# Kernel optimization log

Hardware: AMD Instinct MI355X
Metric: run time of the kernel (lower is better)

Reference implementation:

```python
import jax, jax.numpy as jnp
import numpy as np

N, E, G = 50000, 400000, 2048
H, C = 4, 64            # heads, hidden per head
IN, ED, TASKS = 29, 6, 12
HC = H * C


def setup_inputs() -> dict:
    key = jax.random.key(0)
    ks = jax.random.split(key, 20)
    s = 0.1
    f32 = jnp.float32
    inp = {
        'x': jax.random.normal(ks[0], (N, IN), f32),
        'edge_index': jax.random.randint(ks[1], (2, E), 0, N),
        'edge_attr': jax.random.normal(ks[2], (E, ED), f32),
        'batch': jnp.sort(jax.random.randint(ks[3], (N,), 0, G)),
        # layer 1 (in=29 -> H*C=256)
        'W1': jax.random.normal(ks[4], (IN, HC), f32) * s,
        'as1': jax.random.normal(ks[5], (1, H, C), f32) * s,
        'ad1': jax.random.normal(ks[6], (1, H, C), f32) * s,
        'We1': jax.random.normal(ks[7], (ED, HC), f32) * s,
        'ae1': jax.random.normal(ks[8], (1, H, C), f32) * s,
        'b1': jnp.zeros((HC,), f32),
        # layer 2 (in=256 -> 256)
        'W2': jax.random.normal(ks[9], (HC, HC), f32) * s,
        'as2': jax.random.normal(ks[10], (1, H, C), f32) * s,
        'ad2': jax.random.normal(ks[11], (1, H, C), f32) * s,
        'We2': jax.random.normal(ks[12], (ED, HC), f32) * s,
        'ae2': jax.random.normal(ks[13], (1, H, C), f32) * s,
        'b2': jnp.zeros((HC,), f32),
        # readout linear (256 -> 12)
        'Wl': jax.random.normal(ks[14], (HC, TASKS), f32) * s,
        'bl': jnp.zeros((TASKS,), f32),
    }
    return inp


def _gat_conv(x, src, dst, eattr, W, a_src, a_dst, We, a_e, b):
    """PyG GATConv, concat=True, leaky_relu slope 0.2, self-loops already appended."""
    h = (x @ W).reshape(N, H, C)                      # [N,H,C]
    al_s = jnp.sum(h * a_src, axis=-1)                # [N,H]
    al_d = jnp.sum(h * a_dst, axis=-1)                # [N,H]
    he = (eattr @ We).reshape(-1, H, C)               # [Etot,H,C]
    al_e = jnp.sum(he * a_e, axis=-1)                 # [Etot,H]
    alpha = al_s[src] + al_d[dst] + al_e              # [Etot,H]
    alpha = jax.nn.leaky_relu(alpha, negative_slope=0.2)
    # segment softmax over incoming edges of each dst node
    amax = jax.ops.segment_max(alpha, dst, num_segments=N)
    ex = jnp.exp(alpha - amax[dst])
    denom = jax.ops.segment_sum(ex, dst, num_segments=N)
    alpha = ex / (denom[dst] + 1e-16)
    msg = h[src] * alpha[:, :, None]                  # [Etot,H,C]
    out = jax.ops.segment_sum(msg, dst, num_segments=N)
    return out.reshape(N, HC) + b


def reference(x, edge_index, edge_attr, batch,
              W1, as1, ad1, We1, ae1, b1,
              W2, as2, ad2, We2, ae2, b2, Wl, bl):
    # add self-loops with edge_attr fill = mean over existing edges (PyG default)
    loop = jnp.arange(N)
    src = jnp.concatenate([edge_index[0], loop])
    dst = jnp.concatenate([edge_index[1], loop])
    mean_e = jnp.mean(edge_attr, axis=0, keepdims=True)
    eattr = jnp.concatenate([edge_attr, jnp.broadcast_to(mean_e, (N, ED))], axis=0)

    h = _gat_conv(x, src, dst, eattr, W1, as1, ad1, We1, ae1, b1)
    h = jax.nn.relu(h)
    h = _gat_conv(h, src, dst, eattr, W2, as2, ad2, We2, ae2, b2)
    h = jax.nn.relu(h)

    # global mean pool over graphs
    sums = jax.ops.segment_sum(h, batch, num_segments=G)      # [G,HC]
    cnt = jax.ops.segment_sum(jnp.ones((N,), h.dtype), batch, num_segments=G)
    pooled = sums / jnp.maximum(cnt, 1.0)[:, None]
    return pooled @ Wl + bl
```

## Files before the change

kernel.cpp:

```cpp
#include <hip/hip_runtime.h>
#include <math.h>

static constexpr int NN = 50000;
static constexpr int EE = 400000;
static constexpr int GG = 2048;
static constexpr int TASKS = 12;

typedef __attribute__((ext_vector_type(8))) short short8;
typedef __attribute__((ext_vector_type(4))) float floatx4;

__device__ __forceinline__ unsigned short f2bf(float f) {
  unsigned u = __float_as_uint(f);
  u = u + 0x7fffu + ((u >> 16) & 1u);
  return (unsigned short)(u >> 16);
}
__device__ __forceinline__ float bflo(unsigned u) { return __uint_as_float(u << 16); }
__device__ __forceinline__ float bfhi(unsigned u) { return __uint_as_float(u & 0xffff0000u); }

static constexpr int NBDEG = (EE + 255) / 256;
static constexpr int NBMEAN = 256;
static constexpr int NBX = (NN * 4 + 255) / 256;
static constexpr int NW1 = 32;
static constexpr int NW2 = 256;
__global__ void k_pre(const int* __restrict__ dst, const float* __restrict__ ea,
                      const float* __restrict__ x, const float* __restrict__ W1,
                      const float* __restrict__ W2, int* __restrict__ deg,
                      float* __restrict__ msum, unsigned short* __restrict__ xb,
                      unsigned short* __restrict__ w1t, unsigned short* __restrict__ w2t) {
  const int b = blockIdx.x;
  const int t = threadIdx.x;
  if (b < NBDEG) {
    int e = b * 256 + t;
    if (e < EE) atomicAdd(&deg[dst[e]], 1);
  } else if (b < NBDEG + NBMEAN) {
    float s[6] = {0, 0, 0, 0, 0, 0};
    for (int e = (b - NBDEG) * 256 + t; e < EE; e += NBMEAN * 256) {
#pragma unroll
      for (int d = 0; d < 6; d++) s[d] += ea[(size_t)e * 6 + d];
    }
    __shared__ float ls[6];
    if (t < 6) ls[t] = 0.f;
    __syncthreads();
#pragma unroll
    for (int d = 0; d < 6; d++) atomicAdd(&ls[d], s[d]);
    __syncthreads();
    if (t < 6) atomicAdd(&msum[t], ls[t]);
  } else if (b < NBDEG + NBMEAN + NBX) {
    int i = (b - NBDEG - NBMEAN) * 256 + t;
    if (i < NN * 4) {
      int n = i >> 2, seg = i & 3;
      unsigned short v[8];
#pragma unroll
      for (int j = 0; j < 8; j++) {
        int k = seg * 8 + j;
        v[j] = (k < 29) ? f2bf(x[(size_t)n * 29 + k]) : (unsigned short)0;
      }
      *(short8*)(xb + (size_t)n * 32 + seg * 8) = *(short8*)v;
    }
  } else if (b < NBDEG + NBMEAN + NBX + NW1) {
    int i = (b - NBDEG - NBMEAN - NBX) * 256 + t;
    int row = i >> 5, k = i & 31;
    unsigned short v = (k < 29) ? f2bf(W1[(size_t)k * 256 + row]) : (unsigned short)0;
    w1t[((row >> 4) * 4 + (k >> 3)) * 128 + (row & 15) * 8 + (k & 7)] = v;
  } else {
    int i = (b - NBDEG - NBMEAN - NBX - NW1) * 256 + t;
    int row = i >> 8, k = i & 255;
    w2t[((row >> 4) * 32 + (k >> 3)) * 128 + (row & 15) * 8 + (k & 7)] = f2bf(W2[(size_t)k * 256 + row]);
  }
}

static constexpr int NBS = (NN + 255) / 256;

__global__ void k_scan1(const int* __restrict__ deg, int* __restrict__ rowptr,
                        int* __restrict__ bsums, const float* __restrict__ We1,
                        const float* __restrict__ ae1, const float* __restrict__ We2,
                        const float* __restrict__ ae2, const float* __restrict__ msum,
                        float* __restrict__ p1, float* __restrict__ p2) {
  const int t = threadIdx.x;
  if (blockIdx.x >= NBS) {
    const int layer = blockIdx.x - NBS;
    const float* We = layer ? We2 : We1;
    const float* ae = layer ? ae2 : ae1;
    float* params = layer ? p2 : p1;
    __shared__ float vsh[24];
    if (t < 24) {
      int d = t >> 2, h = t & 3;
      float s = 0.f;
      for (int c = 0; c < 64; c++) s += We[d * 256 + h * 64 + c] * ae[h * 64 + c];
      vsh[t] = s;
      params[t] = s;
    }
    __syncthreads();
    if (t < 4) {
      float s = 0.f;
      const float invE = 1.0f / (float)EE;
#pragma unroll
      for (int d = 0; d < 6; d++) s += (msum[d] * invE) * vsh[d * 4 + t];
      params[24 + t] = s;
    }
    return;
  }
  __shared__ int sh[256];
  int i = blockIdx.x * 256 + t;
  int v = (i < NN) ? deg[i] : 0;
  sh[t] = v;
  __syncthreads();
  for (int off = 1; off < 256; off <<= 1) {
    int tv = (t >= off) ? sh[t - off] : 0;
    __syncthreads();
    sh[t] += tv;
    __syncthreads();
  }
  if (i < NN) rowptr[i] = sh[t] - v;
  if (t == 255) bsums[blockIdx.x] = sh[255];
}

__global__ void k_scan23(int* __restrict__ rowptr, const int* __restrict__ bsums, int nb) {
  __shared__ int sh[256];
  const int t = threadIdx.x;
  sh[t] = (t < nb) ? bsums[t] : 0;
  __syncthreads();
  for (int off = 1; off < 256; off <<= 1) {
    int tv = (t >= off) ? sh[t - off] : 0;
    __syncthreads();
    sh[t] += tv;
    __syncthreads();
  }
  const int add = (blockIdx.x == 0) ? 0 : sh[blockIdx.x - 1];
  int i = blockIdx.x * 256 + t;
  if (i < NN) rowptr[i] += add;
  if (i == 0) rowptr[NN] = EE;
}

template <int KP>
__device__ __forceinline__ void gemm_body(
    int bx, const unsigned short* __restrict__ A, const unsigned short* __restrict__ Bt,
    const float* __restrict__ a_s, const float* __restrict__ a_d,
    unsigned short* __restrict__ Y, float* __restrict__ als, float* __restrict__ ald, int M) {
  __shared__ __align__(16) unsigned short Ash[64 * KP];
  const int tid = threadIdx.x;
  const int lane = tid & 63;
  const int w = tid >> 6;
  const int l15 = lane & 15;
  const int quad = lane >> 4;
  const int row0 = bx * 64;

  constexpr int STEPS = (64 * KP * 2) / (256 * 16);
  {
    const char* Ab = (const char*)(A + (size_t)row0 * KP);
    uint4 stg[STEPS];
#pragma unroll
    for (int s = 0; s < STEPS; s++) stg[s] = *(const uint4*)(Ab + s * 4096 + tid * 16);
#pragma unroll
    for (int s = 0; s < STEPS; s++) {
      int o = s * 4096 + tid * 16;
      int row = o / (KP * 2);
      *(uint4*)((char*)Ash + (o ^ ((row & 7) << 4))) = stg[s];
    }
  }

  floatx4 acc[4][4];
#pragma unroll
  for (int i = 0; i < 4; i++)
#pragma unroll
    for (int j = 0; j < 4; j++) acc[i][j] = {0.f, 0.f, 0.f, 0.f};

  const unsigned short* pb[4];
#pragma unroll
  for (int j = 0; j < 4; j++)
    pb[j] = Bt + (size_t)((w * 4 + j) * (KP / 8) + quad) * 128 + l15 * 8;

  constexpr int NPH = KP / 32;
  short8 bfr[3][4];
#pragma unroll
  for (int j = 0; j < 4; j++) bfr[0][j] = *(const short8*)pb[j];
  if (NPH > 1) {
#pragma unroll
    for (int j = 0; j < 4; j++) {
      pb[j] += 512;
      bfr[1][j] = *(const short8*)pb[j];
    }
  }

  __syncthreads();

  auto ldA = [&](int ph, short8 (&dst)[4]) {
#pragma unroll
    for (int i = 0; i < 4; i++) {
      int lin = (i * 16 + l15) * (KP * 2) + ph * 64 + quad * 16;
      dst[i] = *(const short8*)((const char*)Ash + (lin ^ ((l15 & 7) << 4)));
    }
  };
  short8 af[2][4];
  ldA(0, af[0]);

#pragma unroll
  for (int ph = 0; ph < NPH; ph++) {
    if (ph + 2 < NPH) {
#pragma unroll
      for (int j = 0; j < 4; j++) {
        pb[j] += 512;
        bfr[(ph + 2) % 3][j] = *(const short8*)pb[j];
      }
    }
    if (ph + 1 < NPH) ldA(ph + 1, af[(ph + 1) & 1]);
#pragma unroll
    for (int i = 0; i < 4; i++)
#pragma unroll
      for (int j = 0; j < 4; j++)
        acc[i][j] = __builtin_amdgcn_mfma_f32_16x16x32_bf16(af[ph & 1][i], bfr[ph % 3][j], acc[i][j], 0, 0, 0);
  }
  float asc[4], adc[4];
#pragma unroll
  for (int j = 0; j < 4; j++) {
    asc[j] = a_s[w * 64 + j * 16 + l15];
    adc[j] = a_d[w * 64 + j * 16 + l15];
  }
#pragma unroll
  for (int i = 0; i < 4; i++) {
#pragma unroll
    for (int r = 0; r < 4; r++) {
      const int row = row0 + i * 16 + quad * 4 + r;
      unsigned ub[4];
      float hv[4];
#pragma unroll
      for (int j = 0; j < 4; j++) {
        ub[j] = f2bf(acc[i][j][r]);
        hv[j] = __uint_as_float(ub[j] << 16);
      }
      if (row < M) {
#pragma unroll
        for (int j = 0; j < 4; j++) Y[(size_t)row * 256 + w * 64 + j * 16 + l15] = (unsigned short)ub[j];
      }
      float ps = hv[0] * asc[0] + hv[1] * asc[1] + hv[2] * asc[2] + hv[3] * asc[3];
      float pd = hv[0] * adc[0] + hv[1] * adc[1] + hv[2] * adc[2] + hv[3] * adc[3];
#pragma unroll
      for (int off = 1; off < 16; off <<= 1) {
        ps += __shfl_xor(ps, off, 64);
        pd += __shfl_xor(pd, off, 64);
      }
      if (l15 == 0 && row < M) {
        als[row * 4 + w] = ps;
        ald[row * 4 + w] = pd;
      }
    }
  }
}

static constexpr int GB = (NN + 63) / 64;

__global__ __launch_bounds__(256, 2) void k_scatgemm1(
    const int* __restrict__ ei, const int* __restrict__ rowptr, int* __restrict__ cursor,
    int* __restrict__ csrc, const float* __restrict__ ea,
    const float* __restrict__ p1, const float* __restrict__ p2,
    float* __restrict__ ed1, float* __restrict__ ed2,
    const unsigned short* __restrict__ xb, const unsigned short* __restrict__ w1t,
    const float* __restrict__ as1, const float* __restrict__ ad1,
    unsigned short* __restrict__ hb, float* __restrict__ als, float* __restrict__ ald) {
  const int b = blockIdx.x;
  const int t = threadIdx.x;
  if (b < NBDEG) {
    int e = b * 256 + t;
    if (e >= EE) return;
    int s = ei[e];
    int d = ei[EE + e];
    int p = atomicAdd(&cursor[d], 1);
    int slot = rowptr[d] + p;
    csrc[slot] = s;
    float ed6[6];
#pragma unroll
    for (int d6 = 0; d6 < 6; d6++) ed6[d6] = ea[(size_t)e * 6 + d6];
    float c1[4] = {0.f, 0.f, 0.f, 0.f}, c2[4] = {0.f, 0.f, 0.f, 0.f};
#pragma unroll
    for (int h = 0; h < 4; h++) {
#pragma unroll
      for (int d6 = 0; d6 < 6; d6++) {
        c1[h] += ed6[d6] * p1[d6 * 4 + h];
        c2[h] += ed6[d6] * p2[d6 * 4 + h];
      }
    }
    *(float4*)(ed1 + (size_t)slot * 4) = make_float4(c1[0], c1[1], c1[2], c1[3]);
    *(float4*)(ed2 + (size_t)slot * 4) = make_float4(c2[0], c2[1], c2[2], c2[3]);
  } else {
    gemm_body<32>(b - NBDEG, xb, w1t, as1, ad1, hb, als, ald, NN);
  }
}

__global__ __launch_bounds__(256, 2) void k_gemm2(
    const unsigned short* __restrict__ A, const unsigned short* __restrict__ Bt,
    const float* __restrict__ a_s, const float* __restrict__ a_d,
    unsigned short* __restrict__ Y, float* __restrict__ als, float* __restrict__ ald) {
  gemm_body<256>(blockIdx.x, A, Bt, a_s, a_d, Y, als, ald, NN);
}

__device__ __forceinline__ float leaky02(float x) { return x > 0.f ? x : 0.2f * x; }

__global__ __launch_bounds__(256) void k_agg(
    const unsigned short* __restrict__ hinb, const float* __restrict__ als,
    const float* __restrict__ ald, const int* __restrict__ rowptr, const int* __restrict__ csrc,
    const float* __restrict__ edc, const float* __restrict__ params, const float* __restrict__ bias,
    unsigned short* __restrict__ houtb) {
  const int lane = threadIdx.x & 63;
  const int n = blockIdx.x * 4 + (threadIdx.x >> 6);
  if (n >= NN) return;
  const int half = lane >> 5;
  const int sl = lane & 31;
  const int head = sl >> 3;

  const float aldn = ald[n * 4 + head];
  float acc[8];
  float ssum;
  {
    float slg = leaky02(als[n * 4 + head] + aldn + params[24 + head]);
    float exs = __expf(slg);
    float wgt = (half == 0) ? exs : 0.f;
    ssum = wgt;
    uint4 uv = *(const uint4*)(hinb + (size_t)n * 256 + sl * 8);
    acc[0] = bflo(uv.x) * wgt;
    acc[1] = bfhi(uv.x) * wgt;
    acc[2] = bflo(uv.y) * wgt;
    acc[3] = bfhi(uv.y) * wgt;
    acc[4] = bflo(uv.z) * wgt;
    acc[5] = bfhi(uv.z) * wgt;
    acc[6] = bflo(uv.w) * wgt;
    acc[7] = bfhi(uv.w) * wgt;
  }
  const int end = rowptr[n + 1];
  int s = rowptr[n] + half;
  while (s < end) {
    int sid[4];
    float edv[4];
#pragma unroll
    for (int k = 0; k < 4; k++) {
      const int q = s + 2 * k;
      const bool v = q < end;
      const int idx = v ? q : end - 1;
      sid[k] = csrc[idx];
      edv[k] = v ? edc[(size_t)idx * 4 + head] : 0.f;
    }
    float alv[4];
#pragma unroll
    for (int k = 0; k < 4; k++) alv[k] = als[(size_t)sid[k] * 4 + head];
    uint4 r[4];
#pragma unroll
    for (int k = 0; k < 4; k++) {
      r[k] = make_uint4(0u, 0u, 0u, 0u);
      if (s + 2 * k < end) r[k] = *(const uint4*)(hinb + (size_t)sid[k] * 256 + sl * 8);
    }
#pragma unroll
    for (int k = 0; k < 4; k++) {
      const float ex = (s + 2 * k < end) ? __expf(leaky02(alv[k] + aldn + edv[k])) : 0.f;
      acc[0] += bflo(r[k].x) * ex;
      acc[1] += bfhi(r[k].x) * ex;
      acc[2] += bflo(r[k].y) * ex;
      acc[3] += bfhi(r[k].y) * ex;
      acc[4] += bflo(r[k].z) * ex;
      acc[5] += bfhi(r[k].z) * ex;
      acc[6] += bflo(r[k].w) * ex;
      acc[7] += bfhi(r[k].w) * ex;
      ssum += ex;
    }
    s += 8;
  }
#pragma unroll
  for (int j = 0; j < 8; j++) acc[j] += __shfl_xor(acc[j], 32, 64);
  ssum += __shfl_xor(ssum, 32, 64);
  if (half == 0) {
    const float inv = 1.f / (ssum + 1e-16f);
    float4 b0 = *(const float4*)(bias + sl * 8);
    float4 b1 = *(const float4*)(bias + sl * 8 + 4);
    const float bb[8] = {b0.x, b0.y, b0.z, b0.w, b1.x, b1.y, b1.z, b1.w};
    uint p[4];
#pragma unroll
    for (int j = 0; j < 4; j++) {
      float e0 = fmaxf(acc[2 * j] * inv + bb[2 * j], 0.f);
      float e1 = fmaxf(acc[2 * j + 1] * inv + bb[2 * j + 1], 0.f);
      p[j] = (uint)f2bf(e0) | ((uint)f2bf(e1) << 16);
    }
    *(uint4*)(houtb + (size_t)n * 256 + sl * 8) = make_uint4(p[0], p[1], p[2], p[3]);
  }
}

__global__ __launch_bounds__(256) void k_pool(const unsigned short* __restrict__ hb,
                                              const int* __restrict__ batch,
                                              const float* __restrict__ Wl,
                                              const float* __restrict__ bl,
                                              float* __restrict__ out) {
  int g = blockIdx.x;
  int t = threadIdx.x;
  int lo = 0, hi = NN;
  while (lo < hi) {
    int mid = (lo + hi) >> 1;
    if (batch[mid] < g) lo = mid + 1; else hi = mid;
  }
  int start = lo;
  hi = NN;
  while (lo < hi) {
    int mid = (lo + hi) >> 1;
    if (batch[mid] < g + 1) lo = mid + 1; else hi = mid;
  }
  int end = lo;
  const int mid2 = start + ((end - start) >> 1);
  __shared__ float sp[256], sq[256];
  {
    const int c = t & 127;
    const int hseg = t >> 7;
    const int a = hseg ? mid2 : start;
    const int b = hseg ? end : mid2;
    float s0 = 0.f, s1 = 0.f;
    for (int n2 = a; n2 < b; n2++) {
      uint u = ((const uint*)(hb + (size_t)n2 * 256))[c];
      s0 += bflo(u);
      s1 += bfhi(u);
    }
    float* dst = hseg ? sq : sp;
    dst[2 * c] = s0;
    dst[2 * c + 1] = s1;
  }
  __syncthreads();
  if (t < TASKS) {
    float invc = 1.f / fmaxf((float)(end - start), 1.f);
    float o = bl[t];
    for (int c = 0; c < 256; c++) o += (sp[c] + sq[c]) * invc * Wl[c * 12 + t];
    out[(size_t)g * 12 + t] = o;
  }
}

extern "C" void kernel_launch(void* const* d_in, const int* in_sizes, int n_in,
                              void* d_out, int out_size, void* d_ws, size_t ws_size,
                              hipStream_t stream) {
  const float* x = (const float*)d_in[0];
  const int* ei = (const int*)d_in[1];
  const float* ea = (const float*)d_in[2];
  const int* batch = (const int*)d_in[3];
  const float* W1 = (const float*)d_in[4];
  const float* as1 = (const float*)d_in[5];
  const float* ad1 = (const float*)d_in[6];
  const float* We1 = (const float*)d_in[7];
  const float* ae1 = (const float*)d_in[8];
  const float* b1 = (const float*)d_in[9];
  const float* W2 = (const float*)d_in[10];
  const float* as2 = (const float*)d_in[11];
  const float* ad2 = (const float*)d_in[12];
  const float* We2 = (const float*)d_in[13];
  const float* ae2 = (const float*)d_in[14];
  const float* b2 = (const float*)d_in[15];
  const float* Wl = (const float*)d_in[16];
  const float* bl = (const float*)d_in[17];
  float* out = (float*)d_out;

  char* ws = (char*)d_ws;
  size_t off = 0;
  auto take = [&](size_t bytes) -> char* {
    char* p = ws + off;
    off = (off + bytes + 255) & ~(size_t)255;
    return p;
  };
  float* msum = (float*)take(8 * 4);
  int* deg = (int*)take((size_t)NN * 4);
  int* cursor = (int*)take((size_t)NN * 4);
  size_t zero_end = off;
  int* rowptr = (int*)take((size_t)(NN + 1) * 4);
  int* bsums = (int*)take(256 * 4);
  int* csrc = (int*)take((size_t)EE * 4);
  float* ed1 = (float*)take((size_t)EE * 4 * 4);
  float* ed2 = (float*)take((size_t)EE * 4 * 4);
  float* p1 = (float*)take(32 * 4);
  float* p2 = (float*)take(32 * 4);
  float* als = (float*)take((size_t)NN * 4 * 4);
  float* ald = (float*)take((size_t)NN * 4 * 4);
  unsigned short* hb = (unsigned short*)take((size_t)NN * 256 * 2);
  unsigned short* ab = (unsigned short*)take((size_t)NN * 256 * 2);
  unsigned short* xb = (unsigned short*)take((size_t)NN * 32 * 2);
  unsigned short* w1t = (unsigned short*)take((size_t)256 * 32 * 2);
  unsigned short* w2t = (unsigned short*)take((size_t)256 * 256 * 2);
  (void)ws_size;

  hipMemsetAsync(ws, 0, zero_end, stream);

  k_pre<<<NBDEG + NBMEAN + NBX + NW1 + NW2, 256, 0, stream>>>(ei + EE, ea, x, W1, W2,
                                                              deg, msum, xb, w1t, w2t);
  k_scan1<<<NBS + 2, 256, 0, stream>>>(deg, rowptr, bsums, We1, ae1, We2, ae2, msum, p1, p2);
  k_scan23<<<NBS, 256, 0, stream>>>(rowptr, bsums, NBS);

  k_scatgemm1<<<NBDEG + GB, 256, 0, stream>>>(ei, rowptr, cursor, csrc, ea, p1, p2,
                                              ed1, ed2, xb, w1t, as1, ad1, hb, als, ald);

  k_agg<<<NN / 4, 256, 0, stream>>>(hb, als, ald, rowptr, csrc, ed1, p1, b1, ab);

  k_gemm2<<<GB, 256, 0, stream>>>(ab, w2t, as2, ad2, hb, als, ald);
  k_agg<<<NN / 4, 256, 0, stream>>>(hb, als, ald, rowptr, csrc, ed2, p2, b2, ab);

  k_pool<<<GG, 256, 0, stream>>>(ab, batch, Wl, bl, out);
}
```

Before: 286.8 us.

## Compute edge attention terms on the fly in aggregation instead of precomputing

The scatter kernel now stores a packed (source, original edge id) pair per CSR slot. It no longer projects edge attributes into per-slot per-head attention terms for both layers. The aggregation kernel loads the six raw edge-attribute floats by edge id and dots them with per-head projection parameters held in registers. This removes writing and re-reading two per-edge term arrays, but adds random-order gathers of the edge-attribute array in each aggregation pass and a little extra arithmetic per edge.

```diff
diff --git a/kernel.cpp b/kernel.cpp
--- a/kernel.cpp
+++ b/kernel.cpp
@@ -251,9 +251,7 @@
 
 __global__ __launch_bounds__(256, 2) void k_scatgemm1(
     const int* __restrict__ ei, const int* __restrict__ rowptr, int* __restrict__ cursor,
-    int* __restrict__ csrc, const float* __restrict__ ea,
-    const float* __restrict__ p1, const float* __restrict__ p2,
-    float* __restrict__ ed1, float* __restrict__ ed2,
+    int2* __restrict__ cse,
     const unsigned short* __restrict__ xb, const unsigned short* __restrict__ w1t,
     const float* __restrict__ as1, const float* __restrict__ ad1,
     unsigned short* __restrict__ hb, float* __restrict__ als, float* __restrict__ ald) {
@@ -266,21 +264,7 @@
     int d = ei[EE + e];
     int p = atomicAdd(&cursor[d], 1);
     int slot = rowptr[d] + p;
-    csrc[slot] = s;
-    float ed6[6];
-#pragma unroll
-    for (int d6 = 0; d6 < 6; d6++) ed6[d6] = ea[(size_t)e * 6 + d6];
-    float c1[4] = {0.f, 0.f, 0.f, 0.f}, c2[4] = {0.f, 0.f, 0.f, 0.f};
-#pragma unroll
-    for (int h = 0; h < 4; h++) {
-#pragma unroll
-      for (int d6 = 0; d6 < 6; d6++) {
-        c1[h] += ed6[d6] * p1[d6 * 4 + h];
-        c2[h] += ed6[d6] * p2[d6 * 4 + h];
-      }
-    }
-    *(float4*)(ed1 + (size_t)slot * 4) = make_float4(c1[0], c1[1], c1[2], c1[3]);
-    *(float4*)(ed2 + (size_t)slot * 4) = make_float4(c2[0], c2[1], c2[2], c2[3]);
+    cse[slot] = make_int2(s, e);
   } else {
     gemm_body<32>(b - NBDEG, xb, w1t, as1, ad1, hb, als, ald, NN);
   }
@@ -297,8 +281,8 @@
 
 __global__ __launch_bounds__(256) void k_agg(
     const unsigned short* __restrict__ hinb, const float* __restrict__ als,
-    const float* __restrict__ ald, const int* __restrict__ rowptr, const int* __restrict__ csrc,
-    const float* __restrict__ edc, const float* __restrict__ params, const float* __restrict__ bias,
+    const float* __restrict__ ald, const int* __restrict__ rowptr, const int2* __restrict__ cse,
+    const float* __restrict__ ea, const float* __restrict__ params, const float* __restrict__ bias,
     unsigned short* __restrict__ houtb) {
   const int lane = threadIdx.x & 63;
   const int n = blockIdx.x * 4 + (threadIdx.x >> 6);
@@ -306,6 +290,10 @@
   const int half = lane >> 5;
   const int sl = lane & 31;
   const int head = sl >> 3;
+
+  float pp[6];
+#pragma unroll
+  for (int d = 0; d < 6; d++) pp[d] = params[d * 4 + head];
 
   const float aldn = ald[n * 4 + head];
   float acc[8];
@@ -328,19 +316,27 @@
   const int end = rowptr[n + 1];
   int s = rowptr[n] + half;
   while (s < end) {
-    int sid[4];
-    float edv[4];
+    int sid[4], eid[4];
 #pragma unroll
     for (int k = 0; k < 4; k++) {
       const int q = s + 2 * k;
       const bool v = q < end;
       const int idx = v ? q : end - 1;
-      sid[k] = csrc[idx];
-      edv[k] = v ? edc[(size_t)idx * 4 + head] : 0.f;
+      int2 m = cse[idx];
+      sid[k] = m.x;
+      eid[k] = m.y;
     }
     float alv[4];
 #pragma unroll
     for (int k = 0; k < 4; k++) alv[k] = als[(size_t)sid[k] * 4 + head];
+    float2 er[4][3];
+#pragma unroll
+    for (int k = 0; k < 4; k++) {
+      const float* ep = ea + (size_t)eid[k] * 6;
+      er[k][0] = *(const float2*)ep;
+      er[k][1] = *(const float2*)(ep + 2);
+      er[k][2] = *(const float2*)(ep + 4);
+    }
     uint4 r[4];
 #pragma unroll
     for (int k = 0; k < 4; k++) {
@@ -349,7 +345,9 @@
     }
 #pragma unroll
     for (int k = 0; k < 4; k++) {
-      const float ex = (s + 2 * k < end) ? __expf(leaky02(alv[k] + aldn + edv[k])) : 0.f;
+      float edc = er[k][0].x * pp[0] + er[k][0].y * pp[1] + er[k][1].x * pp[2] +
+                  er[k][1].y * pp[3] + er[k][2].x * pp[4] + er[k][2].y * pp[5];
+      const float ex = (s + 2 * k < end) ? __expf(leaky02(alv[k] + aldn + edc)) : 0.f;
       acc[0] += bflo(r[k].x) * ex;
       acc[1] += bfhi(r[k].x) * ex;
       acc[2] += bflo(r[k].y) * ex;
@@ -462,9 +460,7 @@
   size_t zero_end = off;
   int* rowptr = (int*)take((size_t)(NN + 1) * 4);
   int* bsums = (int*)take(256 * 4);
-  int* csrc = (int*)take((size_t)EE * 4);
-  float* ed1 = (float*)take((size_t)EE * 4 * 4);
-  float* ed2 = (float*)take((size_t)EE * 4 * 4);
+  int2* cse = (int2*)take((size_t)EE * 8);
   float* p1 = (float*)take(32 * 4);
   float* p2 = (float*)take(32 * 4);
   float* als = (float*)take((size_t)NN * 4 * 4);
@@ -483,13 +479,13 @@
   k_scan1<<<NBS + 2, 256, 0, stream>>>(deg, rowptr, bsums, We1, ae1, We2, ae2, msum, p1, p2);
   k_scan23<<<NBS, 256, 0, stream>>>(rowptr, bsums, NBS);
 
-  k_scatgemm1<<<NBDEG + GB, 256, 0, stream>>>(ei, rowptr, cursor, csrc, ea, p1, p2,
-                                              ed1, ed2, xb, w1t, as1, ad1, hb, als, ald);
-
-  k_agg<<<NN / 4, 256, 0, stream>>>(hb, als, ald, rowptr, csrc, ed1, p1, b1, ab);
+  k_scatgemm1<<<NBDEG + GB, 256, 0, stream>>>(ei, rowptr, cursor, cse,
+                                              xb, w1t, as1, ad1, hb, als, ald);
+
+  k_agg<<<NN / 4, 256, 0, stream>>>(hb, als, ald, rowptr, cse, ea, p1, b1, ab);
 
   k_gemm2<<<GB, 256, 0, stream>>>(ab, w2t, as2, ad2, hb, als, ald);
-  k_agg<<<NN / 4, 256, 0, stream>>>(hb, als, ald, rowptr, csrc, ed2, p2, b2, ab);
+  k_agg<<<NN / 4, 256, 0, stream>>>(hb, als, ald, rowptr, cse, ea, p2, b2, ab);
 
   k_pool<<<GG, 256, 0, stream>>>(ab, batch, Wl, bl, out);
 }
```

New measurement: 307.8 us. +7.3%, slower.
